# Kernel optimization log

Hardware: AMD Instinct MI355X
Metric: run time of the kernel (lower is better)

## Reference

```python
import jax, jax.numpy as jnp
import numpy as np

NUM_HEADS = 16
EMBED_DIM = 1024
HEAD_DIM = EMBED_DIM // NUM_HEADS


def setup_inputs() -> dict:
    key = jax.random.key(0)
    kq, kk, kv, kw, kb = jax.random.split(key, 5)
    B, S, D = 2, 2048, EMBED_DIM
    bound = 1.0 / np.sqrt(D)
    return {
        "query": jax.random.normal(kq, (B, S, D), dtype=jnp.float32),
        "key": jax.random.normal(kk, (B, S, D), dtype=jnp.float32),
        "value": jax.random.normal(kv, (B, S, D), dtype=jnp.float32),
        "W_out": jax.random.uniform(kw, (D, D), minval=-bound, maxval=bound, dtype=jnp.float32),
        "b_out": jax.random.uniform(kb, (D,), minval=-bound, maxval=bound, dtype=jnp.float32),
        "prelu_a": jnp.array(0.25, dtype=jnp.float32),
    }


def reference(query, key, value, W_out, b_out, prelu_a):
    B, S, D = query.shape
    # Note: the original forward never applies q/k/v linear layers, only reshape.
    q = query.reshape(B, S, NUM_HEADS, HEAD_DIM)  # b s h d
    k = key.reshape(B, S, NUM_HEADS, HEAD_DIM)
    v = value.reshape(B, S, NUM_HEADS, HEAD_DIM)
    scale = 1.0 / np.sqrt(HEAD_DIM).astype(np.float32)
    scores = jnp.einsum("bqhd,bkhd->bhqk", q, k) * scale  # [B,H,S,S]
    attn = jax.nn.softmax(scores, axis=-1)
    out = jnp.einsum("bhqk,bkhd->bqhd", attn, v).reshape(B, S, D)
    out = out @ W_out.T + b_out  # torch Linear: x @ W.T + b
    # dropout is identity in eval mode; PReLU with single scalar param
    out = jnp.where(out >= 0, out, prelu_a * out)
    return out
```

## Files before the change

kernel.cpp:

```cpp
#include <hip/hip_runtime.h>
#include <hip/hip_bf16.h>

typedef __attribute__((ext_vector_type(8))) short bf16x8;
typedef __attribute__((ext_vector_type(4))) float f32x4;

#define S_LEN 2048
#define EMB   1024
#define NH    16
#define HD    64

__device__ inline int swz(int row, int chunk) {
  return row * 64 + ((chunk ^ (row & 7)) << 3);
}

__device__ inline int kperm(int s) {
  return (s & 0x23) | ((s & 0x04) << 2) | ((s & 0x18) >> 1);
}

__device__ inline uint4 cvt8(const float* __restrict__ src, float scale) {
  float4 f0 = ((const float4*)src)[0];
  float4 f1 = ((const float4*)src)[1];
  __hip_bfloat16 t[8];
  t[0] = __float2bfloat16(f0.x * scale);
  t[1] = __float2bfloat16(f0.y * scale);
  t[2] = __float2bfloat16(f0.z * scale);
  t[3] = __float2bfloat16(f0.w * scale);
  t[4] = __float2bfloat16(f1.x * scale);
  t[5] = __float2bfloat16(f1.y * scale);
  t[6] = __float2bfloat16(f1.z * scale);
  t[7] = __float2bfloat16(f1.w * scale);
  return *(uint4*)t;
}

__global__ __launch_bounds__(256)
void prep(const float* __restrict__ K, const float* __restrict__ V,
          const float* __restrict__ W,
          __hip_bfloat16* __restrict__ Kb, __hip_bfloat16* __restrict__ Vt,
          __hip_bfloat16* __restrict__ Wb) {
  const int tid = threadIdx.x;
  if (blockIdx.z == 2) {
    const int widx = blockIdx.y * 32 + blockIdx.x;
    const int i = (widx * 256 + tid) * 8;
    *(uint4*)(Wb + i) = cvt8(W + i, 1.0f);
    return;
  }
  __shared__ float vt[64 * 65];
  const int st = blockIdx.x, h = blockIdx.y, b = blockIdx.z;
  const size_t srcbase = ((size_t)(b * S_LEN + st * 64)) * EMB + h * HD;
  const size_t kvb = ((size_t)(b * NH + h) * S_LEN + st * 64) * HD;
  const size_t vtb = ((size_t)(b * NH + h) * HD) * S_LEN + st * 64;

  for (int c = tid; c < 512; c += 256) {
    const int r = c >> 3, c8 = (c & 7) * 8;
    *(uint4*)(Kb + kvb + r * HD + c8) = cvt8(K + srcbase + (size_t)r * EMB + c8, 1.0f);
    const float* vsrc = V + srcbase + (size_t)r * EMB + c8;
    float4 a = ((const float4*)vsrc)[0];
    float4 d4 = ((const float4*)vsrc)[1];
    float tv[8] = {a.x, a.y, a.z, a.w, d4.x, d4.y, d4.z, d4.w};
    #pragma unroll
    for (int j = 0; j < 8; ++j) vt[r * 65 + c8 + j] = tv[j];
  }
  __syncthreads();
  for (int c = tid; c < 512; c += 256) {
    const int d = c >> 3, s8 = (c & 7) * 8;
    __hip_bfloat16 t[8];
    #pragma unroll
    for (int j = 0; j < 8; ++j)
      t[j] = __float2bfloat16(vt[(s8 + j) * 65 + d]);
    *(uint4*)(Vt + vtb + (size_t)d * S_LEN + s8) = *(uint4*)t;
  }
}

__global__ __launch_bounds__(512, 4)
void attn_fwd(const float* __restrict__ Q,
              const __hip_bfloat16* __restrict__ Kb,
              const __hip_bfloat16* __restrict__ Vt,
              __hip_bfloat16* __restrict__ O)
{
  __shared__ __align__(16) __hip_bfloat16 qs[128 * 64];
  __shared__ __align__(16) __hip_bfloat16 ks[2][64 * 64];
  __shared__ __align__(16) __hip_bfloat16 vs[2][64 * 64];

  const int qt   = blockIdx.x;
  const int h    = blockIdx.y;
  const int b    = blockIdx.z;
  const int tid  = threadIdx.x;
  const int wave = tid >> 6;
  const int lane = tid & 63;
  const int ln   = lane & 15;
  const int qd   = lane >> 4;

  const size_t baseQ = ((size_t)(b * S_LEN + qt * 128)) * EMB + h * HD;
  const size_t kvb   = ((size_t)(b * NH + h) * S_LEN) * HD;
  const size_t vtb   = ((size_t)(b * NH + h) * HD) * S_LEN;

  const int r0 = tid >> 3, cc = tid & 7;
  const int kpos = swz(kperm(r0), cc);
  const int vpos = swz(r0, cc);

  uint4 kreg = *(const uint4*)(Kb + kvb + (size_t)r0 * HD + cc * 8);
  uint4 vreg = *(const uint4*)(Vt + vtb + (size_t)r0 * S_LEN + cc * 8);

  const float qscale = 0.125f * 1.44269504088896f;
  #pragma unroll
  for (int i = 0; i < 2; ++i) {
    const int c = tid + 512 * i, row = c >> 3, ch = c & 7;
    *(uint4*)&qs[swz(row, ch)] = cvt8(Q + baseQ + (size_t)row * EMB + ch * 8, qscale);
  }
  *(uint4*)&ks[0][kpos] = kreg;
  *(uint4*)&vs[0][vpos] = vreg;
  kreg = *(const uint4*)(Kb + kvb + (size_t)(64 + r0) * HD + cc * 8);
  vreg = *(const uint4*)(Vt + vtb + (size_t)r0 * S_LEN + 64 + cc * 8);
  __syncthreads();

  bf16x8 aq[2];
  #pragma unroll
  for (int kh = 0; kh < 2; ++kh)
    aq[kh] = *(const bf16x8*)&qs[swz(wave * 16 + ln, kh * 4 + qd)];

  f32x4 oacc[4] = {};
  float lsum = 0.f;

  for (int kt = 0; kt < S_LEN / 64; ++kt) {
    const int cur = kt & 1;
    if (kt + 1 < S_LEN / 64) {
      *(uint4*)&ks[1 - cur][kpos] = kreg;
      *(uint4*)&vs[1 - cur][vpos] = vreg;
      if (kt + 2 < S_LEN / 64) {
        kreg = *(const uint4*)(Kb + kvb + (size_t)((kt + 2) * 64 + r0) * HD + cc * 8);
        vreg = *(const uint4*)(Vt + vtb + (size_t)r0 * S_LEN + (kt + 2) * 64 + cc * 8);
      }
    }

    f32x4 sf[4];
    #pragma unroll
    for (int kt16 = 0; kt16 < 4; ++kt16) {
      bf16x8 ak0 = *(const bf16x8*)&ks[cur][swz(kt16 * 16 + ln, qd)];
      bf16x8 ak1 = *(const bf16x8*)&ks[cur][swz(kt16 * 16 + ln, 4 + qd)];
      f32x4 acc = {};
      acc = __builtin_amdgcn_mfma_f32_16x16x32_bf16(ak0, aq[0], acc, 0, 0, 0);
      acc = __builtin_amdgcn_mfma_f32_16x16x32_bf16(ak1, aq[1], acc, 0, 0, 0);
      sf[kt16] = acc;
    }

    bf16x8 ap[2];
    #pragma unroll
    for (int t = 0; t < 2; ++t)
      #pragma unroll
      for (int j = 0; j < 8; ++j) {
        const float p = exp2f(sf[t * 2 + (j >> 2)][j & 3]);
        lsum += p;
        __hip_bfloat16 hb = __float2bfloat16(p);
        ap[t][j] = *(short*)&hb;
      }

    #pragma unroll
    for (int t = 0; t < 2; ++t)
      #pragma unroll
      for (int dn = 0; dn < 4; ++dn) {
        bf16x8 bv = *(const bf16x8*)&vs[cur][swz(dn * 16 + ln, t * 4 + qd)];
        oacc[dn] = __builtin_amdgcn_mfma_f32_16x16x32_bf16(ap[t], bv, oacc[dn], 0, 0, 0);
      }

    __syncthreads();
  }

  lsum += __shfl_xor(lsum, 16);
  lsum += __shfl_xor(lsum, 32);
  #pragma unroll
  for (int r = 0; r < 4; ++r) {
    const float inv = 1.f / __shfl(lsum, qd * 4 + r);
    const int row = wave * 16 + qd * 4 + r;
    #pragma unroll
    for (int dn = 0; dn < 4; ++dn)
      O[baseQ + (size_t)row * EMB + dn * 16 + ln] =
          __float2bfloat16(oacc[dn][r] * inv);
  }
}

__global__ __launch_bounds__(256, 2)
void proj_prelu(const __hip_bfloat16* __restrict__ X,
                const __hip_bfloat16* __restrict__ Wb,
                const float* __restrict__ Bv,
                const float* __restrict__ Pa,
                float* __restrict__ Out)
{
  __shared__ __align__(16) __hip_bfloat16 xs[2][128 * 64];
  __shared__ __align__(16) __hip_bfloat16 wsm[2][128 * 64];

  const int m0   = blockIdx.x * 128;
  const int n0   = blockIdx.y * 128;
  const int tid  = threadIdx.x;
  const int wave = tid >> 6;
  const int wm   = wave >> 1;
  const int wn   = wave & 1;
  const int lane = tid & 63;
  const int ln   = lane & 15;
  const int qd   = lane >> 4;

  const int r0 = tid >> 3, cc = tid & 7;

  f32x4 acc[16] = {};

  uint4 xg0, xg1, xg2, xg3, wg0, wg1, wg2, wg3;
  #define LOADK(ko)                                                        \
    xg0 = *(const uint4*)(X  + (size_t)(m0 + r0     ) * EMB + (ko) + cc * 8); \
    xg1 = *(const uint4*)(X  + (size_t)(m0 + r0 + 32) * EMB + (ko) + cc * 8); \
    xg2 = *(const uint4*)(X  + (size_t)(m0 + r0 + 64) * EMB + (ko) + cc * 8); \
    xg3 = *(const uint4*)(X  + (size_t)(m0 + r0 + 96) * EMB + (ko) + cc * 8); \
    wg0 = *(const uint4*)(Wb + (size_t)(n0 + r0     ) * EMB + (ko) + cc * 8); \
    wg1 = *(const uint4*)(Wb + (size_t)(n0 + r0 + 32) * EMB + (ko) + cc * 8); \
    wg2 = *(const uint4*)(Wb + (size_t)(n0 + r0 + 64) * EMB + (ko) + cc * 8); \
    wg3 = *(const uint4*)(Wb + (size_t)(n0 + r0 + 96) * EMB + (ko) + cc * 8)
  #define STORELDS(buf)                                                    \
    *(uint4*)&xs [buf][swz(r0,      cc)] = xg0;                            \
    *(uint4*)&xs [buf][swz(r0 + 32, cc)] = xg1;                            \
    *(uint4*)&xs [buf][swz(r0 + 64, cc)] = xg2;                            \
    *(uint4*)&xs [buf][swz(r0 + 96, cc)] = xg3;                            \
    *(uint4*)&wsm[buf][swz(r0,      cc)] = wg0;                            \
    *(uint4*)&wsm[buf][swz(r0 + 32, cc)] = wg1;                            \
    *(uint4*)&wsm[buf][swz(r0 + 64, cc)] = wg2;                            \
    *(uint4*)&wsm[buf][swz(r0 + 96, cc)] = wg3

  LOADK(0);
  STORELDS(0);
  LOADK(64);
  __syncthreads();

  for (int kt = 0; kt < EMB / 64; ++kt) {
    const int cur = kt & 1;
    if (kt + 1 < EMB / 64) {
      STORELDS(1 - cur);
      if (kt + 2 < EMB / 64) {
        LOADK((kt + 2) * 64);
      }
    }

    #pragma unroll
    for (int ks2 = 0; ks2 < 2; ++ks2) {
      bf16x8 ax0 = *(const bf16x8*)&xs[cur][swz(wm * 64 +  0 + ln, ks2 * 4 + qd)];
      bf16x8 ax1 = *(const bf16x8*)&xs[cur][swz(wm * 64 + 16 + ln, ks2 * 4 + qd)];
      bf16x8 ax2 = *(const bf16x8*)&xs[cur][swz(wm * 64 + 32 + ln, ks2 * 4 + qd)];
      bf16x8 ax3 = *(const bf16x8*)&xs[cur][swz(wm * 64 + 48 + ln, ks2 * 4 + qd)];
      bf16x8 bw0 = *(const bf16x8*)&wsm[cur][swz(wn * 64 +  0 + ln, ks2 * 4 + qd)];
      bf16x8 bw1 = *(const bf16x8*)&wsm[cur][swz(wn * 64 + 16 + ln, ks2 * 4 + qd)];
      bf16x8 bw2 = *(const bf16x8*)&wsm[cur][swz(wn * 64 + 32 + ln, ks2 * 4 + qd)];
      bf16x8 bw3 = *(const bf16x8*)&wsm[cur][swz(wn * 64 + 48 + ln, ks2 * 4 + qd)];
      acc[ 0] = __builtin_amdgcn_mfma_f32_16x16x32_bf16(ax0, bw0, acc[ 0], 0, 0, 0);
      acc[ 1] = __builtin_amdgcn_mfma_f32_16x16x32_bf16(ax0, bw1, acc[ 1], 0, 0, 0);
      acc[ 2] = __builtin_amdgcn_mfma_f32_16x16x32_bf16(ax0, bw2, acc[ 2], 0, 0, 0);
      acc[ 3] = __builtin_amdgcn_mfma_f32_16x16x32_bf16(ax0, bw3, acc[ 3], 0, 0, 0);
      acc[ 4] = __builtin_amdgcn_mfma_f32_16x16x32_bf16(ax1, bw0, acc[ 4], 0, 0, 0);
      acc[ 5] = __builtin_amdgcn_mfma_f32_16x16x32_bf16(ax1, bw1, acc[ 5], 0, 0, 0);
      acc[ 6] = __builtin_amdgcn_mfma_f32_16x16x32_bf16(ax1, bw2, acc[ 6], 0, 0, 0);
      acc[ 7] = __builtin_amdgcn_mfma_f32_16x16x32_bf16(ax1, bw3, acc[ 7], 0, 0, 0);
      acc[ 8] = __builtin_amdgcn_mfma_f32_16x16x32_bf16(ax2, bw0, acc[ 8], 0, 0, 0);
      acc[ 9] = __builtin_amdgcn_mfma_f32_16x16x32_bf16(ax2, bw1, acc[ 9], 0, 0, 0);
      acc[10] = __builtin_amdgcn_mfma_f32_16x16x32_bf16(ax2, bw2, acc[10], 0, 0, 0);
      acc[11] = __builtin_amdgcn_mfma_f32_16x16x32_bf16(ax2, bw3, acc[11], 0, 0, 0);
      acc[12] = __builtin_amdgcn_mfma_f32_16x16x32_bf16(ax3, bw0, acc[12], 0, 0, 0);
      acc[13] = __builtin_amdgcn_mfma_f32_16x16x32_bf16(ax3, bw1, acc[13], 0, 0, 0);
      acc[14] = __builtin_amdgcn_mfma_f32_16x16x32_bf16(ax3, bw2, acc[14], 0, 0, 0);
      acc[15] = __builtin_amdgcn_mfma_f32_16x16x32_bf16(ax3, bw3, acc[15], 0, 0, 0);
    }
    __syncthreads();
  }

  const float a = Pa[0];
  #pragma unroll
  for (int mf = 0; mf < 4; ++mf) {
    #pragma unroll
    for (int nf = 0; nf < 4; ++nf) {
      const float bn = Bv[n0 + wn * 64 + nf * 16 + ln];
      #pragma unroll
      for (int r = 0; r < 4; ++r) {
        float y = acc[mf * 4 + nf][r] + bn;
        y = (y >= 0.f) ? y : a * y;
        Out[(size_t)(m0 + wm * 64 + mf * 16 + qd * 4 + r) * EMB +
            n0 + wn * 64 + nf * 16 + ln] = y;
      }
    }
  }
  #undef LOADK
  #undef STORELDS
}

extern "C" void kernel_launch(void* const* d_in, const int* in_sizes, int n_in,
                              void* d_out, int out_size, void* d_ws, size_t ws_size,
                              hipStream_t stream) {
  const float* Q  = (const float*)d_in[0];
  const float* K  = (const float*)d_in[1];
  const float* V  = (const float*)d_in[2];
  const float* W  = (const float*)d_in[3];
  const float* Bb = (const float*)d_in[4];
  const float* Pa = (const float*)d_in[5];
  float* Out = (float*)d_out;

  char* ws = (char*)d_ws;
  __hip_bfloat16* Xws = (__hip_bfloat16*)(ws);
  __hip_bfloat16* Kb  = (__hip_bfloat16*)(ws + (8u  << 20));
  __hip_bfloat16* Vt  = (__hip_bfloat16*)(ws + (16u << 20));
  __hip_bfloat16* Wb  = (__hip_bfloat16*)(ws + (24u << 20));

  prep      <<<dim3(S_LEN / 64, NH, 3), 256, 0, stream>>>(K, V, W, Kb, Vt, Wb);
  attn_fwd  <<<dim3(S_LEN / 128, NH, 2), 512, 0, stream>>>(Q, Kb, Vt, Xws);
  proj_prelu<<<dim3(2 * S_LEN / 128, EMB / 128), 256, 0, stream>>>(Xws, Wb, Bb, Pa, Out);
}
```

Measured before the change: 166.6 us.

## Double KV tile to 128 keys and compute softmax row sums via MFMA

The attention kernel now processes 128 keys per iteration instead of 64, doubling the K/V shared-memory tiles and using a wider swizzle for the transposed V tile. This halves the number of loop iterations and block-wide barriers. The scalar row-sum accumulation and its final shuffles are replaced by an MFMA of the bf16 probabilities against a vector of ones, which moves the sum onto the matrix unit but now adds bf16-rounded values. LDS use per block roughly doubles, which may reduce occupancy, and register pressure rises.

```diff
diff --git a/kernel.cpp b/kernel.cpp
--- a/kernel.cpp
+++ b/kernel.cpp
@@ -11,6 +11,10 @@
 
 __device__ inline int swz(int row, int chunk) {
   return row * 64 + ((chunk ^ (row & 7)) << 3);
+}
+
+__device__ inline int swz128(int row, int chunk) {
+  return row * 128 + ((chunk ^ (row & 15)) << 3);
 }
 
 __device__ inline int kperm(int s) {
@@ -78,8 +82,8 @@
               __hip_bfloat16* __restrict__ O)
 {
   __shared__ __align__(16) __hip_bfloat16 qs[128 * 64];
-  __shared__ __align__(16) __hip_bfloat16 ks[2][64 * 64];
-  __shared__ __align__(16) __hip_bfloat16 vs[2][64 * 64];
+  __shared__ __align__(16) __hip_bfloat16 ks[2][128 * 64];
+  __shared__ __align__(16) __hip_bfloat16 vs[2][64 * 128];
 
   const int qt   = blockIdx.x;
   const int h    = blockIdx.y;
@@ -95,11 +99,16 @@
   const size_t vtb   = ((size_t)(b * NH + h) * HD) * S_LEN;
 
   const int r0 = tid >> 3, cc = tid & 7;
-  const int kpos = swz(kperm(r0), cc);
-  const int vpos = swz(r0, cc);
-
-  uint4 kreg = *(const uint4*)(Kb + kvb + (size_t)r0 * HD + cc * 8);
-  uint4 vreg = *(const uint4*)(Vt + vtb + (size_t)r0 * S_LEN + cc * 8);
+  const int kpos0 = swz(kperm(r0), cc);
+  const int kpos1 = kpos0 + 64 * 64;
+  const int vr0 = tid >> 4, vch = tid & 15;
+  const int vpos0 = swz128(vr0, vch);
+  const int vpos1 = vpos0 + 32 * 128;
+
+  uint4 kreg0 = *(const uint4*)(Kb + kvb + (size_t)(r0)       * HD + cc * 8);
+  uint4 kreg1 = *(const uint4*)(Kb + kvb + (size_t)(64 + r0)  * HD + cc * 8);
+  uint4 vreg0 = *(const uint4*)(Vt + vtb + (size_t)vr0        * S_LEN + vch * 8);
+  uint4 vreg1 = *(const uint4*)(Vt + vtb + (size_t)(vr0 + 32) * S_LEN + vch * 8);
 
   const float qscale = 0.125f * 1.44269504088896f;
   #pragma unroll
@@ -107,10 +116,14 @@
     const int c = tid + 512 * i, row = c >> 3, ch = c & 7;
     *(uint4*)&qs[swz(row, ch)] = cvt8(Q + baseQ + (size_t)row * EMB + ch * 8, qscale);
   }
-  *(uint4*)&ks[0][kpos] = kreg;
-  *(uint4*)&vs[0][vpos] = vreg;
-  kreg = *(const uint4*)(Kb + kvb + (size_t)(64 + r0) * HD + cc * 8);
-  vreg = *(const uint4*)(Vt + vtb + (size_t)r0 * S_LEN + 64 + cc * 8);
+  *(uint4*)&ks[0][kpos0] = kreg0;
+  *(uint4*)&ks[0][kpos1] = kreg1;
+  *(uint4*)&vs[0][vpos0] = vreg0;
+  *(uint4*)&vs[0][vpos1] = vreg1;
+  kreg0 = *(const uint4*)(Kb + kvb + (size_t)(128 + r0)      * HD + cc * 8);
+  kreg1 = *(const uint4*)(Kb + kvb + (size_t)(192 + r0)      * HD + cc * 8);
+  vreg0 = *(const uint4*)(Vt + vtb + (size_t)vr0        * S_LEN + 128 + vch * 8);
+  vreg1 = *(const uint4*)(Vt + vtb + (size_t)(vr0 + 32) * S_LEN + 128 + vch * 8);
   __syncthreads();
 
   bf16x8 aq[2];
@@ -118,58 +131,71 @@
   for (int kh = 0; kh < 2; ++kh)
     aq[kh] = *(const bf16x8*)&qs[swz(wave * 16 + ln, kh * 4 + qd)];
 
+  bf16x8 ones;
+  #pragma unroll
+  for (int j = 0; j < 8; ++j) ones[j] = (short)0x3F80;
+
   f32x4 oacc[4] = {};
-  float lsum = 0.f;
-
-  for (int kt = 0; kt < S_LEN / 64; ++kt) {
+  f32x4 lacc = {};
+
+  for (int kt = 0; kt < S_LEN / 128; ++kt) {
     const int cur = kt & 1;
-    if (kt + 1 < S_LEN / 64) {
-      *(uint4*)&ks[1 - cur][kpos] = kreg;
-      *(uint4*)&vs[1 - cur][vpos] = vreg;
-      if (kt + 2 < S_LEN / 64) {
-        kreg = *(const uint4*)(Kb + kvb + (size_t)((kt + 2) * 64 + r0) * HD + cc * 8);
-        vreg = *(const uint4*)(Vt + vtb + (size_t)r0 * S_LEN + (kt + 2) * 64 + cc * 8);
-      }
-    }
-
-    f32x4 sf[4];
-    #pragma unroll
-    for (int kt16 = 0; kt16 < 4; ++kt16) {
-      bf16x8 ak0 = *(const bf16x8*)&ks[cur][swz(kt16 * 16 + ln, qd)];
-      bf16x8 ak1 = *(const bf16x8*)&ks[cur][swz(kt16 * 16 + ln, 4 + qd)];
-      f32x4 acc = {};
-      acc = __builtin_amdgcn_mfma_f32_16x16x32_bf16(ak0, aq[0], acc, 0, 0, 0);
-      acc = __builtin_amdgcn_mfma_f32_16x16x32_bf16(ak1, aq[1], acc, 0, 0, 0);
-      sf[kt16] = acc;
-    }
-
-    bf16x8 ap[2];
-    #pragma unroll
-    for (int t = 0; t < 2; ++t)
+    if (kt + 1 < S_LEN / 128) {
+      *(uint4*)&ks[1 - cur][kpos0] = kreg0;
+      *(uint4*)&ks[1 - cur][kpos1] = kreg1;
+      *(uint4*)&vs[1 - cur][vpos0] = vreg0;
+      *(uint4*)&vs[1 - cur][vpos1] = vreg1;
+      if (kt + 2 < S_LEN / 128) {
+        const int kb2 = (kt + 2) * 128;
+        kreg0 = *(const uint4*)(Kb + kvb + (size_t)(kb2 + r0)       * HD + cc * 8);
+        kreg1 = *(const uint4*)(Kb + kvb + (size_t)(kb2 + 64 + r0)  * HD + cc * 8);
+        vreg0 = *(const uint4*)(Vt + vtb + (size_t)vr0        * S_LEN + kb2 + vch * 8);
+        vreg1 = *(const uint4*)(Vt + vtb + (size_t)(vr0 + 32) * S_LEN + kb2 + vch * 8);
+      }
+    }
+
+    bf16x8 ap[4];
+    #pragma unroll
+    for (int half = 0; half < 2; ++half) {
+      f32x4 sf[4];
       #pragma unroll
-      for (int j = 0; j < 8; ++j) {
-        const float p = exp2f(sf[t * 2 + (j >> 2)][j & 3]);
-        lsum += p;
-        __hip_bfloat16 hb = __float2bfloat16(p);
-        ap[t][j] = *(short*)&hb;
-      }
-
-    #pragma unroll
-    for (int t = 0; t < 2; ++t)
+      for (int k16 = 0; k16 < 4; ++k16) {
+        const int krow = (half * 4 + k16) * 16 + ln;
+        bf16x8 ak0 = *(const bf16x8*)&ks[cur][swz(krow, qd)];
+        bf16x8 ak1 = *(const bf16x8*)&ks[cur][swz(krow, 4 + qd)];
+        f32x4 acc = {};
+        acc = __builtin_amdgcn_mfma_f32_16x16x32_bf16(ak0, aq[0], acc, 0, 0, 0);
+        acc = __builtin_amdgcn_mfma_f32_16x16x32_bf16(ak1, aq[1], acc, 0, 0, 0);
+        sf[k16] = acc;
+      }
+      #pragma unroll
+      for (int t2 = 0; t2 < 2; ++t2)
+        #pragma unroll
+        for (int j = 0; j < 8; ++j) {
+          const float p = exp2f(sf[t2 * 2 + (j >> 2)][j & 3]);
+          __hip_bfloat16 hb = __float2bfloat16(p);
+          ap[half * 2 + t2][j] = *(short*)&hb;
+        }
+    }
+
+    #pragma unroll
+    for (int t = 0; t < 4; ++t)
+      lacc = __builtin_amdgcn_mfma_f32_16x16x32_bf16(ap[t], ones, lacc, 0, 0, 0);
+
+    #pragma unroll
+    for (int t = 0; t < 4; ++t)
       #pragma unroll
       for (int dn = 0; dn < 4; ++dn) {
-        bf16x8 bv = *(const bf16x8*)&vs[cur][swz(dn * 16 + ln, t * 4 + qd)];
+        bf16x8 bv = *(const bf16x8*)&vs[cur][swz128(dn * 16 + ln, t * 4 + qd)];
         oacc[dn] = __builtin_amdgcn_mfma_f32_16x16x32_bf16(ap[t], bv, oacc[dn], 0, 0, 0);
       }
 
     __syncthreads();
   }
 
-  lsum += __shfl_xor(lsum, 16);
-  lsum += __shfl_xor(lsum, 32);
   #pragma unroll
   for (int r = 0; r < 4; ++r) {
-    const float inv = 1.f / __shfl(lsum, qd * 4 + r);
+    const float inv = 1.f / lacc[r];
     const int row = wave * 16 + qd * 4 + r;
     #pragma unroll
     for (int dn = 0; dn < 4; ++dn)
```

Result: slower. 170.4 us (+2.3%).
